# Performance work log

Hardware: AMD Instinct MI355X
Metric: run time of the kernel (lower is better)

Reference implementation:

```python
import jax, jax.numpy as jnp
import numpy as np
import math

B, T, H = 2, 1024, 2048
NH, NKV, HD = 8, 2, 256
S = 4           # altup_num_inputs
FF = 8192       # intermediate_size
LR = 64         # laurel_rank
EPS = 1e-6
ROPE_THETA = 1e6


def _ln(x, w):
    # Gemma3nRMSNorm in this repo: fp32 mean-subtract then F.layer_norm (no bias)
    x32 = x.astype(jnp.float32)
    xc = x32 - x32.mean(-1, keepdims=True)
    var = (xc * xc).mean(-1, keepdims=True)
    return (xc * jax.lax.rsqrt(var + EPS) * w.astype(jnp.float32)).astype(x.dtype)


def _rotate_half(x):
    x1, x2 = jnp.split(x, 2, axis=-1)
    return jnp.concatenate((-x2, x1), axis=-1)


def _rope(x, cos, sin):  # x: [B,nh,T,hd]; cos/sin: [B,T,hd]
    return x * cos[:, None] + _rotate_half(x) * sin[:, None]


def setup_inputs() -> dict:
    key = jax.random.key(0)
    ks = jax.random.split(key, 24)

    def w(k, shape, scale=0.02):
        return jax.random.normal(k, shape, jnp.float32) * scale

    hidden_states = jax.random.normal(ks[0], (S, B, T, H), jnp.float32)

    # real rotary embeddings
    inv_freq = 1.0 / (ROPE_THETA ** (np.arange(0, HD, 2, dtype=np.float64) / HD))
    freqs = np.arange(T, dtype=np.float64)[:, None] * inv_freq[None, :]
    emb = np.concatenate([freqs, freqs], axis=-1)  # [T,HD]
    cos = jnp.broadcast_to(jnp.asarray(np.cos(emb), jnp.float32)[None], (B, T, HD))
    sin = jnp.broadcast_to(jnp.asarray(np.sin(emb), jnp.float32)[None], (B, T, HD))

    return {
        "hidden_states": hidden_states, "cos": cos, "sin": sin,
        "wq": w(ks[1], (NH * HD, H)), "wk": w(ks[2], (NKV * HD, H)),
        "wv": w(ks[3], (NKV * HD, H)), "wo": w(ks[4], (H, NH * HD)),
        "q_norm_w": jnp.ones((HD,), jnp.float32), "k_norm_w": jnp.ones((HD,), jnp.float32),
        "input_ln_w": jnp.ones((H,), jnp.float32), "post_attn_ln_w": jnp.ones((H,), jnp.float32),
        "pre_ffw_ln_w": jnp.ones((H,), jnp.float32), "post_ffw_ln_w": jnp.ones((H,), jnp.float32),
        "gate_w": w(ks[5], (FF, H)), "up_w": w(ks[6], (FF, H)), "down_w": w(ks[7], (H, FF)),
        "laurel_left_w": w(ks[8], (LR, H)), "laurel_right_w": w(ks[9], (H, LR)),
        "laurel_norm_w": jnp.ones((H,), jnp.float32),
        "router_norm_w": jnp.ones((H,), jnp.float32),
        "router_w": w(ks[10], (S, H)),
        "pred_coef_w": w(ks[11], (S * S, S)),
        "corr_coef_w": w(ks[12], (S, S)),
        "correct_output_scale": w(ks[13], (H,), 1.0),
    }


def reference(hidden_states, cos, sin, wq, wk, wv, wo, q_norm_w, k_norm_w,
              input_ln_w, post_attn_ln_w, pre_ffw_ln_w, post_ffw_ln_w,
              gate_w, up_w, down_w, laurel_left_w, laurel_right_w, laurel_norm_w,
              router_norm_w, router_w, pred_coef_w, corr_coef_w, correct_output_scale):
    def modalities_of(x):  # router: RMSNorm -> scale -> linear -> tanh
        r = _ln(x, router_norm_w) * (1.0 / H)
        return jnp.tanh((r @ router_w.T).astype(jnp.float32)).astype(x.dtype)

    # ---- AltUp predict ----
    m = modalities_of(hidden_states[0])                      # [B,T,S]
    coefs = (m @ pred_coef_w.T).reshape(B, T, S, S)          # raw [B,T,S_out,S_in]
    # torch: matmul(h.permute(1,2,3,0), coefs.permute(0,1,3,2)) => sum_s h[s]*raw[...,j,s]
    predictions = jnp.einsum('sbth,btjs->jbth', hidden_states, coefs) + hidden_states

    active = predictions[0]
    x_norm = _ln(active, input_ln_w)

    # ---- Laurel block ----
    lau = (x_norm @ laurel_left_w.T) @ laurel_right_w.T
    laurel_out = x_norm + _ln(lau, laurel_norm_w)

    # ---- Attention (GQA, q/k/v norms, rope, scale=1.0) ----
    q = _ln((x_norm @ wq.T).reshape(B, T, NH, HD), q_norm_w).transpose(0, 2, 1, 3)
    q = _rope(q, cos, sin)
    k = _ln((x_norm @ wk.T).reshape(B, T, NKV, HD), k_norm_w).transpose(0, 2, 1, 3)
    k = _rope(k, cos, sin)
    v = _ln((x_norm @ wv.T).reshape(B, T, NKV, HD), jnp.ones((HD,), jnp.float32))
    v = v.transpose(0, 2, 1, 3)
    rep = NH // NKV
    k = jnp.repeat(k, rep, axis=1)
    v = jnp.repeat(v, rep, axis=1)
    scores = jnp.einsum('bhqd,bhkd->bhqk', q, k)             # scaling = 1.0 in Gemma3n
    causal = jnp.tril(jnp.ones((T, T), bool))
    scores = jnp.where(causal, scores, jnp.finfo(jnp.float32).min)
    attn = jax.nn.softmax(scores.astype(jnp.float32), axis=-1).astype(q.dtype)
    out = jnp.einsum('bhqk,bhkd->bhqd', attn, v)
    out = out.transpose(0, 2, 1, 3).reshape(B, T, NH * HD) @ wo.T
    out = _ln(out, post_attn_ln_w)

    attn_gated = active + out
    attn_laurel = (attn_gated + laurel_out) * (1.0 / math.sqrt(2.0))

    # ---- MLP (gelu-tanh gated) ----
    h = _ln(attn_laurel, pre_ffw_ln_w)
    ffw = (jax.nn.gelu(h @ gate_w.T, approximate=True) * (h @ up_w.T)) @ down_w.T
    ffw = _ln(ffw, post_ffw_ln_w)
    activated = attn_laurel + ffw

    # ---- AltUp correct ----
    mc = modalities_of(activated)                            # [B,T,S]
    innovation = activated - predictions[0]                  # [B,T,H]
    ccoefs = (mc @ corr_coef_w.T) + 1.0                      # [B,T,S]
    corrected = innovation[None] * ccoefs.transpose(2, 0, 1)[..., None] + predictions

    # scale_corrected_output on the active stream (altup_correct_scale=True)
    first = (corrected[0] * correct_output_scale).astype(corrected.dtype)
    corrected = corrected.at[0].set(first)
    return corrected
```

## Files before the change

kernel.cpp:

```cpp
#include <hip/hip_runtime.h>
#include <hip/hip_bf16.h>
#include <math.h>

#define B_   2
#define T_   1024
#define H_   2048
#define NH_  8
#define NKV_ 2
#define HD_  256
#define S_   4
#define FF_  8192
#define LR_  64
#define ROWS_ (B_*T_)
#define EPS_ 1e-6f

typedef __attribute__((ext_vector_type(8))) __bf16 bf16x8;
typedef __attribute__((ext_vector_type(4))) float floatx4;
typedef __attribute__((ext_vector_type(8))) unsigned short ushort8v;

__device__ __forceinline__ unsigned short f2bf(float f) {
    unsigned int u = __float_as_uint(f);
    return (unsigned short)((u + 0x7FFFu + ((u >> 16) & 1u)) >> 16);
}

__device__ __forceinline__ void gl_lds16(const void* g, void* l) {
    __builtin_amdgcn_global_load_lds(
        (const __attribute__((address_space(1))) void*)g,
        (__attribute__((address_space(3))) void*)l, 16, 0, 0);
}

__device__ __forceinline__ float block_sum(float v) {
    __shared__ float s4[4];
    #pragma unroll
    for (int o = 32; o > 0; o >>= 1) v += __shfl_down(v, o, 64);
    int lane = threadIdx.x & 63;
    int w    = threadIdx.x >> 6;
    __syncthreads();
    if (lane == 0) s4[w] = v;
    __syncthreads();
    return s4[0] + s4[1] + s4[2] + s4[3];
}

__device__ __forceinline__ float block_max(float v) {
    __shared__ float s4m[4];
    #pragma unroll
    for (int o = 32; o > 0; o >>= 1) v = fmaxf(v, __shfl_down(v, o, 64));
    int lane = threadIdx.x & 63;
    int w    = threadIdx.x >> 6;
    __syncthreads();
    if (lane == 0) s4m[w] = v;
    __syncthreads();
    return fmaxf(fmaxf(s4m[0], s4m[1]), fmaxf(s4m[2], s4m[3]));
}

__global__ __launch_bounds__(256) void cvt_bf16(
    const float* __restrict__ in, unsigned short* __restrict__ out, int n)
{
    int i = (blockIdx.x * 256 + threadIdx.x) * 8;
    if (i >= n) return;
    float4 v0 = *reinterpret_cast<const float4*>(in + i);
    float4 v1 = *reinterpret_cast<const float4*>(in + i + 4);
    ushort8v o;
    o[0] = f2bf(v0.x); o[1] = f2bf(v0.y); o[2] = f2bf(v0.z); o[3] = f2bf(v0.w);
    o[4] = f2bf(v1.x); o[5] = f2bf(v1.y); o[6] = f2bf(v1.z); o[7] = f2bf(v1.w);
    *reinterpret_cast<ushort8v*>(out + i) = o;
}

__global__ __launch_bounds__(256) void router_kernel(
    const float* __restrict__ x, const float* __restrict__ nw,
    const float* __restrict__ rw, float* __restrict__ mout)
{
    size_t row = blockIdx.x;
    int tid = threadIdx.x;
    const float* xr = x + row * H_;
    float v[8]; float s = 0.f;
    #pragma unroll
    for (int i = 0; i < 8; ++i) { v[i] = xr[i*256 + tid]; s += v[i]; }
    float mu = block_sum(s) * (1.f / H_);
    float ss = 0.f;
    #pragma unroll
    for (int i = 0; i < 8; ++i) { float c = v[i] - mu; ss += c * c; }
    float rstd = rsqrtf(block_sum(ss) * (1.f / H_) + EPS_);
    float n[8];
    #pragma unroll
    for (int i = 0; i < 8; ++i) n[i] = (v[i] - mu) * rstd * nw[i*256 + tid];
    for (int so = 0; so < S_; ++so) {
        float p = 0.f;
        #pragma unroll
        for (int i = 0; i < 8; ++i) p += n[i] * rw[(size_t)so * H_ + i*256 + tid];
        float dot = block_sum(p);
        if (tid == 0) mout[row * S_ + so] = tanhf(dot * (1.f / H_));
    }
}

__global__ __launch_bounds__(256) void predict_kernel(
    const float* __restrict__ hid, const float* __restrict__ m,
    const float* __restrict__ pcw, float* __restrict__ pred)
{
    size_t row = blockIdx.x;
    int tid = threadIdx.x;
    __shared__ float ms[4];
    __shared__ float c[16];
    if (tid < 4) ms[tid] = m[row * S_ + tid];
    __syncthreads();
    if (tid < 16) {
        float s = 0.f;
        #pragma unroll
        for (int i = 0; i < 4; ++i) s += ms[i] * pcw[tid * 4 + i];
        c[tid] = s;
    }
    __syncthreads();
    const size_t STRIDE = (size_t)ROWS_ * H_;
    #pragma unroll
    for (int i = 0; i < 8; ++i) {
        size_t idx = row * H_ + i*256 + tid;
        float h0 = hid[idx];
        float h1 = hid[idx + STRIDE];
        float h2 = hid[idx + 2*STRIDE];
        float h3 = hid[idx + 3*STRIDE];
        float hv[4] = {h0, h1, h2, h3};
        #pragma unroll
        for (int j = 0; j < 4; ++j) {
            float val = hv[j] + h0*c[j*4+0] + h1*c[j*4+1] + h2*c[j*4+2] + h3*c[j*4+3];
            pred[idx + (size_t)j * STRIDE] = val;
        }
    }
}

__global__ __launch_bounds__(256) void ln_residual(
    const float* __restrict__ x, const float* __restrict__ xadd,
    const float* __restrict__ w,
    const float* __restrict__ a1, const float* __restrict__ a2,
    float scale, float* __restrict__ out, unsigned short* __restrict__ outb)
{
    size_t row = blockIdx.x;
    int tid = threadIdx.x;
    const float* xr = x + row * H_;
    const float* xa = xadd ? xadd + row * H_ : nullptr;
    float v[8]; float s = 0.f;
    #pragma unroll
    for (int i = 0; i < 8; ++i) {
        v[i] = xr[i*256 + tid];
        if (xa) v[i] += xa[i*256 + tid];
        s += v[i];
    }
    float mu = block_sum(s) * (1.f / H_);
    float ss = 0.f;
    #pragma unroll
    for (int i = 0; i < 8; ++i) { float c = v[i] - mu; ss += c * c; }
    float rstd = rsqrtf(block_sum(ss) * (1.f / H_) + EPS_);
    #pragma unroll
    for (int i = 0; i < 8; ++i) {
        size_t idx = row * H_ + i*256 + tid;
        float y = (v[i] - mu) * rstd * w[i*256 + tid];
        if (a1) y += a1[idx];
        if (a2) y += a2[idx];
        y *= scale;
        if (out)  out[idx]  = y;
        if (outb) outb[idx] = f2bf(y);
    }
}

#define BM 64
#define BN 64
#define BK 32
#define LDP 68

__global__ __launch_bounds__(256) void gemm_nt(
    const float* __restrict__ A, const float* __restrict__ Bm,
    float* __restrict__ C, int M, int N, int K)
{
    __shared__ float As[BK][LDP];
    __shared__ float Bs[BK][LDP];
    int tid = threadIdx.x;
    int n0 = blockIdx.x * BN;
    int m0 = blockIdx.y * BM;
    int tx = tid & 15, ty = tid >> 4;
    int lrow = tid >> 3;
    int lk   = (tid & 7) << 2;
    float acc[4][4] = {};
    for (int k0 = 0; k0 < K; k0 += BK) {
        #pragma unroll
        for (int r = 0; r < 2; ++r) {
            int row = lrow + r * 32;
            float4 a4 = *reinterpret_cast<const float4*>(&A[(size_t)(m0 + row) * K + k0 + lk]);
            As[lk+0][row] = a4.x; As[lk+1][row] = a4.y; As[lk+2][row] = a4.z; As[lk+3][row] = a4.w;
            float4 b4 = *reinterpret_cast<const float4*>(&Bm[(size_t)(n0 + row) * K + k0 + lk]);
            Bs[lk+0][row] = b4.x; Bs[lk+1][row] = b4.y; Bs[lk+2][row] = b4.z; Bs[lk+3][row] = b4.w;
        }
        __syncthreads();
        #pragma unroll
        for (int k = 0; k < BK; ++k) {
            float4 av = *reinterpret_cast<const float4*>(&As[k][ty << 2]);
            float4 bv = *reinterpret_cast<const float4*>(&Bs[k][tx << 2]);
            float a[4] = {av.x, av.y, av.z, av.w};
            float b[4] = {bv.x, bv.y, bv.z, bv.w};
            #pragma unroll
            for (int i = 0; i < 4; ++i)
                #pragma unroll
                for (int j = 0; j < 4; ++j)
                    acc[i][j] = fmaf(a[i], b[j], acc[i][j]);
        }
        __syncthreads();
    }
    #pragma unroll
    for (int i = 0; i < 4; ++i) {
        float4 o; o.x = acc[i][0]; o.y = acc[i][1]; o.z = acc[i][2]; o.w = acc[i][3];
        *reinterpret_cast<float4*>(&C[(size_t)(m0 + (ty << 2) + i) * N + n0 + (tx << 2)]) = o;
    }
}

__global__ __launch_bounds__(256) void gemm_bf16nt(
    const unsigned short* __restrict__ A, const unsigned short* __restrict__ Bm,
    float* __restrict__ C, float* __restrict__ C2, int M, int N, int K)
{
    __shared__ unsigned short As[8192];
    __shared__ unsigned short Bs[8192];
    int tid = threadIdx.x;
    int lane = tid & 63;
    int wave = tid >> 6;
    int m0 = blockIdx.y * 128, n0 = blockIdx.x * 128;
    int Kper = K / gridDim.z;
    int kbeg = blockIdx.z * Kper;
    int kend = kbeg + Kper;
    int wm = (wave >> 1) * 64;
    int wn = (wave & 1) * 64;
    floatx4 acc[4][4] = {};

    const unsigned short* aG0 = A  + (size_t)(m0 + lane)      * K + wave * 8;
    const unsigned short* aG1 = A  + (size_t)(m0 + 64 + lane) * K + wave * 8;
    const unsigned short* bG0 = Bm + (size_t)(n0 + lane)      * K + wave * 8;
    const unsigned short* bG1 = Bm + (size_t)(n0 + 64 + lane) * K + wave * 8;

    int kc = lane >> 4, mr = lane & 15;

    {
        unsigned short* a = &As[wave * 1024];
        unsigned short* b = &Bs[wave * 1024];
        gl_lds16(aG0 + kbeg, a);
        gl_lds16(aG1 + kbeg, a + 512);
        gl_lds16(bG0 + kbeg, b);
        gl_lds16(bG1 + kbeg, b + 512);
    }
    __syncthreads();
    int cur = 0;
    for (int k0 = kbeg; k0 < kend; k0 += 32) {
        if (k0 + 32 < kend) {
            int nb = (cur ^ 1) * 4096;
            unsigned short* a = &As[nb + wave * 1024];
            unsigned short* b = &Bs[nb + wave * 1024];
            gl_lds16(aG0 + k0 + 32, a);
            gl_lds16(aG1 + k0 + 32, a + 512);
            gl_lds16(bG0 + k0 + 32, b);
            gl_lds16(bG1 + k0 + 32, b + 512);
        }
        int cb = cur * 4096;
        bf16x8 af[4], bfv[4];
        #pragma unroll
        for (int mi = 0; mi < 4; ++mi)
            af[mi] = *reinterpret_cast<const bf16x8*>(&As[cb + kc * 1024 + (wm + mi * 16 + mr) * 8]);
        #pragma unroll
        for (int ni = 0; ni < 4; ++ni)
            bfv[ni] = *reinterpret_cast<const bf16x8*>(&Bs[cb + kc * 1024 + (wn + ni * 16 + mr) * 8]);
        #pragma unroll
        for (int mi = 0; mi < 4; ++mi)
            #pragma unroll
            for (int ni = 0; ni < 4; ++ni)
                acc[mi][ni] = __builtin_amdgcn_mfma_f32_16x16x32_bf16(af[mi], bfv[ni], acc[mi][ni], 0, 0, 0);
        __syncthreads();
        cur ^= 1;
    }
    float* Cout = (blockIdx.z == 0) ? C : C2;
    int quad = lane >> 4;
    #pragma unroll
    for (int mi = 0; mi < 4; ++mi)
        #pragma unroll
        for (int ni = 0; ni < 4; ++ni)
            #pragma unroll
            for (int r = 0; r < 4; ++r)
                Cout[(size_t)(m0 + wm + mi * 16 + quad * 4 + r) * N + n0 + wn + ni * 16 + mr] = acc[mi][ni][r];
}

__global__ __launch_bounds__(256) void gemm_gateup_bf16(
    const unsigned short* __restrict__ A, const unsigned short* __restrict__ G,
    const unsigned short* __restrict__ U, unsigned short* __restrict__ Cbf,
    int M, int N, int K)
{
    __shared__ unsigned short As[8192];
    __shared__ unsigned short Gs[4096];
    __shared__ unsigned short Us[4096];
    int tid = threadIdx.x;
    int lane = tid & 63;
    int wave = tid >> 6;
    int m0 = blockIdx.y * 128, n0 = blockIdx.x * 64;
    floatx4 accg[2][4] = {};
    floatx4 accu[2][4] = {};

    const unsigned short* aG0 = A + (size_t)(m0 + lane)      * K + wave * 8;
    const unsigned short* aG1 = A + (size_t)(m0 + 64 + lane) * K + wave * 8;
    const unsigned short* gG  = G + (size_t)(n0 + lane)      * K + wave * 8;
    const unsigned short* uG  = U + (size_t)(n0 + lane)      * K + wave * 8;

    int kc = lane >> 4, mr = lane & 15;

    {
        gl_lds16(aG0, &As[wave * 1024]);
        gl_lds16(aG1, &As[wave * 1024 + 512]);
        gl_lds16(gG,  &Gs[wave * 512]);
        gl_lds16(uG,  &Us[wave * 512]);
    }
    __syncthreads();
    int cur = 0;
    for (int k0 = 0; k0 < K; k0 += 32) {
        if (k0 + 32 < K) {
            int a_nb = (cur ^ 1) * 4096;
            int g_nb = (cur ^ 1) * 2048;
            gl_lds16(aG0 + k0 + 32, &As[a_nb + wave * 1024]);
            gl_lds16(aG1 + k0 + 32, &As[a_nb + wave * 1024 + 512]);
            gl_lds16(gG + k0 + 32,  &Gs[g_nb + wave * 512]);
            gl_lds16(uG + k0 + 32,  &Us[g_nb + wave * 512]);
        }
        int ab = cur * 4096, gb = cur * 2048;
        bf16x8 af[2], gf[4], uf[4];
        #pragma unroll
        for (int mi = 0; mi < 2; ++mi)
            af[mi] = *reinterpret_cast<const bf16x8*>(&As[ab + kc * 1024 + (wave * 32 + mi * 16 + mr) * 8]);
        #pragma unroll
        for (int ni = 0; ni < 4; ++ni) {
            gf[ni] = *reinterpret_cast<const bf16x8*>(&Gs[gb + kc * 512 + (ni * 16 + mr) * 8]);
            uf[ni] = *reinterpret_cast<const bf16x8*>(&Us[gb + kc * 512 + (ni * 16 + mr) * 8]);
        }
        #pragma unroll
        for (int mi = 0; mi < 2; ++mi)
            #pragma unroll
            for (int ni = 0; ni < 4; ++ni) {
                accg[mi][ni] = __builtin_amdgcn_mfma_f32_16x16x32_bf16(af[mi], gf[ni], accg[mi][ni], 0, 0, 0);
                accu[mi][ni] = __builtin_amdgcn_mfma_f32_16x16x32_bf16(af[mi], uf[ni], accu[mi][ni], 0, 0, 0);
            }
        __syncthreads();
        cur ^= 1;
    }
    int quad = lane >> 4;
    #pragma unroll
    for (int mi = 0; mi < 2; ++mi) {
        int rb = m0 + wave * 32 + mi * 16 + quad * 4;
        #pragma unroll
        for (int ni = 0; ni < 4; ++ni)
            #pragma unroll
            for (int r = 0; r < 4; ++r) {
                float g = accg[mi][ni][r];
                float gl = 0.5f * g * (1.f + tanhf(0.7978845608028654f * (g + 0.044715f * g * g * g)));
                float val = gl * accu[mi][ni][r];
                Cbf[(size_t)(rb + r) * N + n0 + ni * 16 + mr] = f2bf(val);
            }
    }
}

__global__ __launch_bounds__(256) void qkv_norm_rope_fused(
    const float* __restrict__ in, const float* __restrict__ qw,
    const float* __restrict__ kw,
    const float* __restrict__ cs, const float* __restrict__ sn,
    unsigned short* __restrict__ qo, unsigned short* __restrict__ ko,
    unsigned short* __restrict__ vo)
{
    int blk = blockIdx.x;
    int hh = blk % 12;
    int trow = blk / 12;
    int b = trow / T_;
    int t = trow % T_;
    int d = threadIdx.x;
    float x = in[(size_t)trow * 3072 + hh * HD_ + d];
    float mu = block_sum(x) * (1.f / HD_);
    float xc = x - mu;
    float var = block_sum(xc * xc) * (1.f / HD_);
    float wv_ = (hh < 8) ? qw[d] : (hh < 10 ? kw[d] : 1.f);
    float n = xc * rsqrtf(var + EPS_) * wv_;
    __shared__ float buf[HD_];
    buf[d] = n;
    __syncthreads();
    float val = n;
    if (hh < 10) {
        float c = cs[(size_t)trow * HD_ + d];
        float s = sn[(size_t)trow * HD_ + d];
        float other = (d < 128) ? -buf[d + 128] : buf[d - 128];
        val = n * c + other * s;
    }
    if (hh < 8)
        qo[(((size_t)b * NH_ + hh) * T_ + t) * HD_ + d] = f2bf(val);
    else if (hh < 10)
        ko[(((size_t)b * NKV_ + (hh - 8)) * T_ + t) * HD_ + d] = f2bf(val);
    else
        vo[(((size_t)b * NKV_ + (hh - 10)) * HD_ + d) * T_ + t] = f2bf(val);
}

__global__ __launch_bounds__(256) void qk_gemm(
    const unsigned short* __restrict__ Q, const unsigned short* __restrict__ Kt,
    float* __restrict__ S, int head_base)
{
    if (blockIdx.x > blockIdx.y) return;
    int z = blockIdx.z;
    int bh = head_base + z;
    const unsigned short* A  = Q  + (size_t)bh * T_ * HD_;
    const unsigned short* Bm = Kt + (size_t)(bh >> 2) * T_ * HD_;
    float* C = S + (size_t)z * T_ * T_;

    __shared__ unsigned short As[8192];
    __shared__ unsigned short Bs[8192];
    int tid = threadIdx.x;
    int lane = tid & 63;
    int wave = tid >> 6;
    int m0 = blockIdx.y * 128, n0 = blockIdx.x * 128;
    int wm = (wave >> 1) * 64;
    int wn = (wave & 1) * 64;
    floatx4 acc[4][4] = {};

    const unsigned short* aG0 = A  + (size_t)(m0 + lane)      * HD_ + wave * 8;
    const unsigned short* aG1 = A  + (size_t)(m0 + 64 + lane) * HD_ + wave * 8;
    const unsigned short* bG0 = Bm + (size_t)(n0 + lane)      * HD_ + wave * 8;
    const unsigned short* bG1 = Bm + (size_t)(n0 + 64 + lane) * HD_ + wave * 8;

    int kc = lane >> 4, mr = lane & 15;

    {
        gl_lds16(aG0, &As[wave * 1024]);
        gl_lds16(aG1, &As[wave * 1024 + 512]);
        gl_lds16(bG0, &Bs[wave * 1024]);
        gl_lds16(bG1, &Bs[wave * 1024 + 512]);
    }
    __syncthreads();
    int cur = 0;
    for (int k0 = 0; k0 < HD_; k0 += 32) {
        if (k0 + 32 < HD_) {
            int nb = (cur ^ 1) * 4096;
            gl_lds16(aG0 + k0 + 32, &As[nb + wave * 1024]);
            gl_lds16(aG1 + k0 + 32, &As[nb + wave * 1024 + 512]);
            gl_lds16(bG0 + k0 + 32, &Bs[nb + wave * 1024]);
            gl_lds16(bG1 + k0 + 32, &Bs[nb + wave * 1024 + 512]);
        }
        int cb = cur * 4096;
        bf16x8 af[4], bfv[4];
        #pragma unroll
        for (int mi = 0; mi < 4; ++mi)
            af[mi] = *reinterpret_cast<const bf16x8*>(&As[cb + kc * 1024 + (wm + mi * 16 + mr) * 8]);
        #pragma unroll
        for (int ni = 0; ni < 4; ++ni)
            bfv[ni] = *reinterpret_cast<const bf16x8*>(&Bs[cb + kc * 1024 + (wn + ni * 16 + mr) * 8]);
        #pragma unroll
        for (int mi = 0; mi < 4; ++mi)
            #pragma unroll
            for (int ni = 0; ni < 4; ++ni)
                acc[mi][ni] = __builtin_amdgcn_mfma_f32_16x16x32_bf16(af[mi], bfv[ni], acc[mi][ni], 0, 0, 0);
        __syncthreads();
        cur ^= 1;
    }
    int quad = lane >> 4;
    #pragma unroll
    for (int mi = 0; mi < 4; ++mi)
        #pragma unroll
        for (int ni = 0; ni < 4; ++ni)
            #pragma unroll
            for (int r = 0; r < 4; ++r)
                C[(size_t)(m0 + wm + mi * 16 + quad * 4 + r) * T_ + n0 + wn + ni * 16 + mr] = acc[mi][ni][r];
}

__global__ __launch_bounds__(256) void softmax_causal(
    const float* __restrict__ S, unsigned short* __restrict__ P)
{
    int qi = blockIdx.x;
    int g  = blockIdx.y;
    int tid = threadIdx.x;
    int L = qi + 1;
    const float* Srow = S + ((size_t)g * T_ + qi) * T_;
    unsigned short* Prow = P + ((size_t)g * T_ + qi) * T_;
    float v[4];
    float mx = -3.402823466e38f;
    #pragma unroll
    for (int i = 0; i < 4; ++i) {
        int idx = i * 256 + tid;
        v[i] = (idx < L) ? Srow[idx] : -3.402823466e38f;
        mx = fmaxf(mx, v[i]);
    }
    mx = block_max(mx);
    float sm = 0.f;
    float e[4];
    #pragma unroll
    for (int i = 0; i < 4; ++i) {
        int idx = i * 256 + tid;
        e[i] = (idx < L) ? expf(v[i] - mx) : 0.f;
        sm += e[i];
    }
    sm = block_sum(sm);
    float inv = 1.f / sm;
    #pragma unroll
    for (int i = 0; i < 4; ++i)
        Prow[i * 256 + tid] = f2bf(e[i] * inv);
}

__global__ __launch_bounds__(256) void pv_gemm(
    const unsigned short* __restrict__ P, const unsigned short* __restrict__ Vt,
    unsigned short* __restrict__ Out)
{
    int z = blockIdx.z;
    int b = z >> 3;
    int h = z & 7;
    const unsigned short* A  = P  + (size_t)z * T_ * T_;
    const unsigned short* Bm = Vt + (size_t)(z >> 2) * HD_ * T_;

    __shared__ unsigned short As[8192];
    __shared__ unsigned short Bs[8192];
    int tid = threadIdx.x;
    int lane = tid & 63;
    int wave = tid >> 6;
    int m0 = blockIdx.y * 128, n0 = blockIdx.x * 128;
    int Kend = m0 + 128;
    int wm = (wave >> 1) * 64;
    int wn = (wave & 1) * 64;
    floatx4 acc[4][4] = {};

    const unsigned short* aG0 = A  + (size_t)(m0 + lane)      * T_ + wave * 8;
    const unsigned short* aG1 = A  + (size_t)(m0 + 64 + lane) * T_ + wave * 8;
    const unsigned short* bG0 = Bm + (size_t)(n0 + lane)      * T_ + wave * 8;
    const unsigned short* bG1 = Bm + (size_t)(n0 + 64 + lane) * T_ + wave * 8;

    int kc = lane >> 4, mr = lane & 15;

    {
        gl_lds16(aG0, &As[wave * 1024]);
        gl_lds16(aG1, &As[wave * 1024 + 512]);
        gl_lds16(bG0, &Bs[wave * 1024]);
        gl_lds16(bG1, &Bs[wave * 1024 + 512]);
    }
    __syncthreads();
    int cur = 0;
    for (int k0 = 0; k0 < Kend; k0 += 32) {
        if (k0 + 32 < Kend) {
            int nb = (cur ^ 1) * 4096;
            gl_lds16(aG0 + k0 + 32, &As[nb + wave * 1024]);
            gl_lds16(aG1 + k0 + 32, &As[nb + wave * 1024 + 512]);
            gl_lds16(bG0 + k0 + 32, &Bs[nb + wave * 1024]);
            gl_lds16(bG1 + k0 + 32, &Bs[nb + wave * 1024 + 512]);
        }
        int cb = cur * 4096;
        bf16x8 af[4], bfv[4];
        #pragma unroll
        for (int mi = 0; mi < 4; ++mi)
            af[mi] = *reinterpret_cast<const bf16x8*>(&As[cb + kc * 1024 + (wm + mi * 16 + mr) * 8]);
        #pragma unroll
        for (int ni = 0; ni < 4; ++ni)
            bfv[ni] = *reinterpret_cast<const bf16x8*>(&Bs[cb + kc * 1024 + (wn + ni * 16 + mr) * 8]);
        #pragma unroll
        for (int mi = 0; mi < 4; ++mi)
            #pragma unroll
            for (int ni = 0; ni < 4; ++ni)
                acc[mi][ni] = __builtin_amdgcn_mfma_f32_16x16x32_bf16(af[mi], bfv[ni], acc[mi][ni], 0, 0, 0);
        __syncthreads();
        cur ^= 1;
    }
    int quad = lane >> 4;
    #pragma unroll
    for (int mi = 0; mi < 4; ++mi)
        #pragma unroll
        for (int ni = 0; ni < 4; ++ni)
            #pragma unroll
            for (int r = 0; r < 4; ++r) {
                int row = m0 + wm + mi * 16 + quad * 4 + r;
                int col = n0 + wn + ni * 16 + mr;
                Out[((size_t)(b * T_ + row)) * (NH_ * HD_) + h * HD_ + col] =
                    f2bf(acc[mi][ni][r]);
            }
}

__global__ __launch_bounds__(256) void correct_kernel(
    const float* __restrict__ act, const float* __restrict__ pred,
    const float* __restrict__ mc, const float* __restrict__ ccw,
    const float* __restrict__ cscale, float* __restrict__ out)
{
    size_t row = blockIdx.x;
    int tid = threadIdx.x;
    __shared__ float ms[4];
    __shared__ float cc[4];
    if (tid < 4) ms[tid] = mc[row * S_ + tid];
    __syncthreads();
    if (tid < 4) {
        float s = 1.f;
        #pragma unroll
        for (int i = 0; i < 4; ++i) s += ms[i] * ccw[tid * 4 + i];
        cc[tid] = s;
    }
    __syncthreads();
    const size_t STRIDE = (size_t)ROWS_ * H_;
    #pragma unroll
    for (int i = 0; i < 8; ++i) {
        size_t idx = row * H_ + i*256 + tid;
        float a  = act[idx];
        float p0 = pred[idx];
        float inn = a - p0;
        #pragma unroll
        for (int j = 0; j < 4; ++j) {
            float val = inn * cc[j] + pred[idx + (size_t)j * STRIDE];
            if (j == 0) val *= cscale[i*256 + tid];
            out[idx + (size_t)j * STRIDE] = val;
        }
    }
}

extern "C" void kernel_launch(void* const* d_in, const int* in_sizes, int n_in,
                              void* d_out, int out_size, void* d_ws, size_t ws_size,
                              hipStream_t stream)
{
    (void)in_sizes; (void)n_in; (void)out_size; (void)ws_size;
    const float* hidden         = (const float*)d_in[0];
    const float* cosp           = (const float*)d_in[1];
    const float* sinp           = (const float*)d_in[2];
    const float* wq             = (const float*)d_in[3];
    const float* wk             = (const float*)d_in[4];
    const float* wv             = (const float*)d_in[5];
    const float* wo             = (const float*)d_in[6];
    const float* q_norm_w       = (const float*)d_in[7];
    const float* k_norm_w       = (const float*)d_in[8];
    const float* input_ln_w     = (const float*)d_in[9];
    const float* post_attn_ln_w = (const float*)d_in[10];
    const float* pre_ffw_ln_w   = (const float*)d_in[11];
    const float* post_ffw_ln_w  = (const float*)d_in[12];
    const float* gate_w         = (const float*)d_in[13];
    const float* up_w           = (const float*)d_in[14];
    const float* down_w         = (const float*)d_in[15];
    const float* ll_w           = (const float*)d_in[16];
    const float* lr_w           = (const float*)d_in[17];
    const float* laurel_norm_w  = (const float*)d_in[18];
    const float* router_norm_w  = (const float*)d_in[19];
    const float* router_w       = (const float*)d_in[20];
    const float* pred_coef_w    = (const float*)d_in[21];
    const float* corr_coef_w    = (const float*)d_in[22];
    const float* cscale         = (const float*)d_in[23];
    float* outp = (float*)d_out;

    char* base = (char*)d_ws;
    float* pred   = (float*)base;              base += 67108864;
    float* xnorm  = (float*)base;              base += 16777216;
    unsigned short* xnorm_bf = (unsigned short*)base; base += 8388608;
    float* lout   = (float*)base;              base += 16777216;
    float* alaur  = (float*)base;              base += 16777216;
    float* tmpH   = (float*)base;              base += 16777216;
    float* mbuf   = (float*)base;              base += 32768;
    float* mcbuf  = (float*)base;              base += 32768;
    float* ltmp   = (float*)base;              base += 524288;
    char* arena = base;
    unsigned short* qkvw_bf = (unsigned short*)arena;
    float* qkv_pre = (float*)(arena + 12582912);
    unsigned short* Pbuf    = (unsigned short*)arena;
    unsigned short* q_bf    = (unsigned short*)(arena + 37748736);
    unsigned short* k_bf    = (unsigned short*)(arena + 46137344);
    unsigned short* vT_bf   = (unsigned short*)(arena + 48234496);
    unsigned short* attn_bf = (unsigned short*)(arena + 50331648);
    unsigned short* wo_bf   = (unsigned short*)(arena + 58720256);
    float* Sbuf             = (float*)(arena + 67108864);
    unsigned short* gate_bf = (unsigned short*)arena;
    unsigned short* up_bf   = (unsigned short*)(arena + 33554432);
    unsigned short* gu_bf   = (unsigned short*)(arena + 67108864);
    unsigned short* down_bf = gate_bf;
    float* activated = lout;

    router_kernel <<<ROWS_, 256, 0, stream>>>(hidden, router_norm_w, router_w, mbuf);
    predict_kernel<<<ROWS_, 256, 0, stream>>>(hidden, mbuf, pred_coef_w, pred);
    ln_residual   <<<ROWS_, 256, 0, stream>>>(pred, nullptr, input_ln_w, nullptr, nullptr, 1.f, xnorm, xnorm_bf);

    gemm_nt<<<dim3(LR_/BN, ROWS_/BM), 256, 0, stream>>>(xnorm, ll_w, ltmp, ROWS_, LR_, H_);
    gemm_nt<<<dim3(H_/BN,  ROWS_/BM), 256, 0, stream>>>(ltmp, lr_w, tmpH, ROWS_, H_, LR_);
    ln_residual<<<ROWS_, 256, 0, stream>>>(tmpH, nullptr, laurel_norm_w, xnorm, nullptr, 1.f, lout, nullptr);

    cvt_bf16<<<2048, 256, 0, stream>>>(wq, qkvw_bf,            4194304);
    cvt_bf16<<< 512, 256, 0, stream>>>(wk, qkvw_bf + 4194304,  1048576);
    cvt_bf16<<< 512, 256, 0, stream>>>(wv, qkvw_bf + 5242880,  1048576);
    gemm_bf16nt<<<dim3(24, 16, 1), 256, 0, stream>>>(xnorm_bf, qkvw_bf, qkv_pre, nullptr, ROWS_, 3072, H_);
    qkv_norm_rope_fused<<<ROWS_*12, 256, 0, stream>>>(qkv_pre, q_norm_w, k_norm_w, cosp, sinp, q_bf, k_bf, vT_bf);
    cvt_bf16<<<2048, 256, 0, stream>>>(wo, wo_bf, 4194304);
    for (int hb = 0; hb < B_ * NH_; hb += 8) {
        qk_gemm       <<<dim3(8, 8, 8), 256, 0, stream>>>(q_bf, k_bf, Sbuf, hb);
        softmax_causal<<<dim3(T_, 8),   256, 0, stream>>>(Sbuf, Pbuf + (size_t)hb * T_ * T_);
    }
    pv_gemm<<<dim3(2, 8, 16), 256, 0, stream>>>(Pbuf, vT_bf, attn_bf);
    gemm_bf16nt<<<dim3(16, 16, 2), 256, 0, stream>>>(attn_bf, wo_bf, tmpH, xnorm, ROWS_, H_, NH_*HD_);
    ln_residual<<<ROWS_, 256, 0, stream>>>(tmpH, xnorm, post_attn_ln_w, pred, lout, 0.7071067811865475f, alaur, nullptr);

    ln_residual<<<ROWS_, 256, 0, stream>>>(alaur, nullptr, pre_ffw_ln_w, nullptr, nullptr, 1.f, nullptr, xnorm_bf);
    cvt_bf16<<<8192, 256, 0, stream>>>(gate_w, gate_bf, 16777216);
    cvt_bf16<<<8192, 256, 0, stream>>>(up_w,   up_bf,   16777216);
    gemm_gateup_bf16<<<dim3(128, 16), 256, 0, stream>>>(xnorm_bf, gate_bf, up_bf, gu_bf, ROWS_, FF_, H_);
    cvt_bf16<<<8192, 256, 0, stream>>>(down_w, down_bf, 16777216);
    gemm_bf16nt<<<dim3(16, 16, 2), 256, 0, stream>>>(gu_bf, down_bf, tmpH, xnorm, ROWS_, H_, FF_);
    ln_residual<<<ROWS_, 256, 0, stream>>>(tmpH, xnorm, post_ffw_ln_w, alaur, nullptr, 1.f, activated, nullptr);

    router_kernel <<<ROWS_, 256, 0, stream>>>(activated, router_norm_w, router_w, mcbuf);
    correct_kernel<<<ROWS_, 256, 0, stream>>>(activated, pred, mcbuf, corr_coef_w, cscale, outp);
}
```

Measured before the change: 1.183 ms.

## Coalesce global-to-LDS loads with row-major K tiles; widen gate/up GEMM tile

Each GEMM's global-to-LDS loader now reads four consecutive 16-byte chunks of a row per four lanes, where before each lane read a different row. The LDS tile is stored row-major with 32 K-elements per row, and the fragment reads are re-indexed to match. The gate/up GEMM tile grows from 128x64 to 128x128 with a 2x2 wave layout, doubling accumulators per thread and halving the grid. This targets uncoalesced global loads and redundant A-tile reads, at the risk of LDS bank conflicts from the 64-byte row stride and higher register pressure in the gate/up kernel.

Result: faster. 1.116 ms (-5.7%).

```diff
diff --git a/kernel.cpp b/kernel.cpp
--- a/kernel.cpp
+++ b/kernel.cpp
@@ -227,41 +227,37 @@
     int wn = (wave & 1) * 64;
     floatx4 acc[4][4] = {};
 
-    const unsigned short* aG0 = A  + (size_t)(m0 + lane)      * K + wave * 8;
-    const unsigned short* aG1 = A  + (size_t)(m0 + 64 + lane) * K + wave * 8;
-    const unsigned short* bG0 = Bm + (size_t)(n0 + lane)      * K + wave * 8;
-    const unsigned short* bG1 = Bm + (size_t)(n0 + 64 + lane) * K + wave * 8;
+    int lr = lane >> 2;
+    int lc = lane & 3;
+    const unsigned short* aG0 = A  + (size_t)(m0 + wave*16 + lr) * K + lc * 8;
+    const unsigned short* aG1 = aG0 + (size_t)64 * K;
+    const unsigned short* bG0 = Bm + (size_t)(n0 + wave*16 + lr) * K + lc * 8;
+    const unsigned short* bG1 = bG0 + (size_t)64 * K;
 
     int kc = lane >> 4, mr = lane & 15;
 
-    {
-        unsigned short* a = &As[wave * 1024];
-        unsigned short* b = &Bs[wave * 1024];
-        gl_lds16(aG0 + kbeg, a);
-        gl_lds16(aG1 + kbeg, a + 512);
-        gl_lds16(bG0 + kbeg, b);
-        gl_lds16(bG1 + kbeg, b + 512);
-    }
+    gl_lds16(aG0 + kbeg, &As[wave * 512]);
+    gl_lds16(aG1 + kbeg, &As[2048 + wave * 512]);
+    gl_lds16(bG0 + kbeg, &Bs[wave * 512]);
+    gl_lds16(bG1 + kbeg, &Bs[2048 + wave * 512]);
     __syncthreads();
     int cur = 0;
     for (int k0 = kbeg; k0 < kend; k0 += 32) {
         if (k0 + 32 < kend) {
             int nb = (cur ^ 1) * 4096;
-            unsigned short* a = &As[nb + wave * 1024];
-            unsigned short* b = &Bs[nb + wave * 1024];
-            gl_lds16(aG0 + k0 + 32, a);
-            gl_lds16(aG1 + k0 + 32, a + 512);
-            gl_lds16(bG0 + k0 + 32, b);
-            gl_lds16(bG1 + k0 + 32, b + 512);
+            gl_lds16(aG0 + k0 + 32, &As[nb + wave * 512]);
+            gl_lds16(aG1 + k0 + 32, &As[nb + 2048 + wave * 512]);
+            gl_lds16(bG0 + k0 + 32, &Bs[nb + wave * 512]);
+            gl_lds16(bG1 + k0 + 32, &Bs[nb + 2048 + wave * 512]);
         }
         int cb = cur * 4096;
         bf16x8 af[4], bfv[4];
         #pragma unroll
         for (int mi = 0; mi < 4; ++mi)
-            af[mi] = *reinterpret_cast<const bf16x8*>(&As[cb + kc * 1024 + (wm + mi * 16 + mr) * 8]);
+            af[mi] = *reinterpret_cast<const bf16x8*>(&As[cb + (wm + mi * 16 + mr) * 32 + kc * 8]);
         #pragma unroll
         for (int ni = 0; ni < 4; ++ni)
-            bfv[ni] = *reinterpret_cast<const bf16x8*>(&Bs[cb + kc * 1024 + (wn + ni * 16 + mr) * 8]);
+            bfv[ni] = *reinterpret_cast<const bf16x8*>(&Bs[cb + (wn + ni * 16 + mr) * 32 + kc * 8]);
         #pragma unroll
         for (int mi = 0; mi < 4; ++mi)
             #pragma unroll
@@ -287,51 +283,58 @@
     int M, int N, int K)
 {
     __shared__ unsigned short As[8192];
-    __shared__ unsigned short Gs[4096];
-    __shared__ unsigned short Us[4096];
+    __shared__ unsigned short Gs[8192];
+    __shared__ unsigned short Us[8192];
     int tid = threadIdx.x;
     int lane = tid & 63;
     int wave = tid >> 6;
-    int m0 = blockIdx.y * 128, n0 = blockIdx.x * 64;
-    floatx4 accg[2][4] = {};
-    floatx4 accu[2][4] = {};
-
-    const unsigned short* aG0 = A + (size_t)(m0 + lane)      * K + wave * 8;
-    const unsigned short* aG1 = A + (size_t)(m0 + 64 + lane) * K + wave * 8;
-    const unsigned short* gG  = G + (size_t)(n0 + lane)      * K + wave * 8;
-    const unsigned short* uG  = U + (size_t)(n0 + lane)      * K + wave * 8;
+    int m0 = blockIdx.y * 128, n0 = blockIdx.x * 128;
+    int wm  = (wave >> 1) * 64;
+    int wnf = (wave & 1) * 64;
+    floatx4 accg[4][4] = {};
+    floatx4 accu[4][4] = {};
+
+    int lr = lane >> 2;
+    int lc = lane & 3;
+    const unsigned short* aG0 = A + (size_t)(m0 + wave*16 + lr) * K + lc * 8;
+    const unsigned short* aG1 = aG0 + (size_t)64 * K;
+    const unsigned short* gG0 = G + (size_t)(n0 + wave*16 + lr) * K + lc * 8;
+    const unsigned short* gG1 = gG0 + (size_t)64 * K;
+    const unsigned short* uG0 = U + (size_t)(n0 + wave*16 + lr) * K + lc * 8;
+    const unsigned short* uG1 = uG0 + (size_t)64 * K;
 
     int kc = lane >> 4, mr = lane & 15;
 
-    {
-        gl_lds16(aG0, &As[wave * 1024]);
-        gl_lds16(aG1, &As[wave * 1024 + 512]);
-        gl_lds16(gG,  &Gs[wave * 512]);
-        gl_lds16(uG,  &Us[wave * 512]);
-    }
+    gl_lds16(aG0, &As[wave * 512]);
+    gl_lds16(aG1, &As[2048 + wave * 512]);
+    gl_lds16(gG0, &Gs[wave * 512]);
+    gl_lds16(gG1, &Gs[2048 + wave * 512]);
+    gl_lds16(uG0, &Us[wave * 512]);
+    gl_lds16(uG1, &Us[2048 + wave * 512]);
     __syncthreads();
     int cur = 0;
     for (int k0 = 0; k0 < K; k0 += 32) {
         if (k0 + 32 < K) {
-            int a_nb = (cur ^ 1) * 4096;
-            int g_nb = (cur ^ 1) * 2048;
-            gl_lds16(aG0 + k0 + 32, &As[a_nb + wave * 1024]);
-            gl_lds16(aG1 + k0 + 32, &As[a_nb + wave * 1024 + 512]);
-            gl_lds16(gG + k0 + 32,  &Gs[g_nb + wave * 512]);
-            gl_lds16(uG + k0 + 32,  &Us[g_nb + wave * 512]);
-        }
-        int ab = cur * 4096, gb = cur * 2048;
-        bf16x8 af[2], gf[4], uf[4];
-        #pragma unroll
-        for (int mi = 0; mi < 2; ++mi)
-            af[mi] = *reinterpret_cast<const bf16x8*>(&As[ab + kc * 1024 + (wave * 32 + mi * 16 + mr) * 8]);
+            int nb = (cur ^ 1) * 4096;
+            gl_lds16(aG0 + k0 + 32, &As[nb + wave * 512]);
+            gl_lds16(aG1 + k0 + 32, &As[nb + 2048 + wave * 512]);
+            gl_lds16(gG0 + k0 + 32, &Gs[nb + wave * 512]);
+            gl_lds16(gG1 + k0 + 32, &Gs[nb + 2048 + wave * 512]);
+            gl_lds16(uG0 + k0 + 32, &Us[nb + wave * 512]);
+            gl_lds16(uG1 + k0 + 32, &Us[nb + 2048 + wave * 512]);
+        }
+        int cb = cur * 4096;
+        bf16x8 af[4], gf[4], uf[4];
+        #pragma unroll
+        for (int mi = 0; mi < 4; ++mi)
+            af[mi] = *reinterpret_cast<const bf16x8*>(&As[cb + (wm + mi * 16 + mr) * 32 + kc * 8]);
         #pragma unroll
         for (int ni = 0; ni < 4; ++ni) {
-            gf[ni] = *reinterpret_cast<const bf16x8*>(&Gs[gb + kc * 512 + (ni * 16 + mr) * 8]);
-            uf[ni] = *reinterpret_cast<const bf16x8*>(&Us[gb + kc * 512 + (ni * 16 + mr) * 8]);
-        }
-        #pragma unroll
-        for (int mi = 0; mi < 2; ++mi)
+            gf[ni] = *reinterpret_cast<const bf16x8*>(&Gs[cb + (wnf + ni * 16 + mr) * 32 + kc * 8]);
+            uf[ni] = *reinterpret_cast<const bf16x8*>(&Us[cb + (wnf + ni * 16 + mr) * 32 + kc * 8]);
+        }
+        #pragma unroll
+        for (int mi = 0; mi < 4; ++mi)
             #pragma unroll
             for (int ni = 0; ni < 4; ++ni) {
                 accg[mi][ni] = __builtin_amdgcn_mfma_f32_16x16x32_bf16(af[mi], gf[ni], accg[mi][ni], 0, 0, 0);
@@ -342,8 +345,8 @@
     }
     int quad = lane >> 4;
     #pragma unroll
-    for (int mi = 0; mi < 2; ++mi) {
-        int rb = m0 + wave * 32 + mi * 16 + quad * 4;
+    for (int mi = 0; mi < 4; ++mi) {
+        int rb = m0 + wm + mi * 16 + quad * 4;
         #pragma unroll
         for (int ni = 0; ni < 4; ++ni)
             #pragma unroll
@@ -351,7 +354,7 @@
                 float g = accg[mi][ni][r];
                 float gl = 0.5f * g * (1.f + tanhf(0.7978845608028654f * (g + 0.044715f * g * g * g)));
                 float val = gl * accu[mi][ni][r];
-                Cbf[(size_t)(rb + r) * N + n0 + ni * 16 + mr] = f2bf(val);
+                Cbf[(size_t)(rb + r) * N + n0 + wnf + ni * 16 + mr] = f2bf(val);
             }
     }
 }
@@ -414,37 +417,37 @@
     int wn = (wave & 1) * 64;
     floatx4 acc[4][4] = {};
 
-    const unsigned short* aG0 = A  + (size_t)(m0 + lane)      * HD_ + wave * 8;
-    const unsigned short* aG1 = A  + (size_t)(m0 + 64 + lane) * HD_ + wave * 8;
-    const unsigned short* bG0 = Bm + (size_t)(n0 + lane)      * HD_ + wave * 8;
-    const unsigned short* bG1 = Bm + (size_t)(n0 + 64 + lane) * HD_ + wave * 8;
+    int lr = lane >> 2;
+    int lc = lane & 3;
+    const unsigned short* aG0 = A  + (size_t)(m0 + wave*16 + lr) * HD_ + lc * 8;
+    const unsigned short* aG1 = aG0 + (size_t)64 * HD_;
+    const unsigned short* bG0 = Bm + (size_t)(n0 + wave*16 + lr) * HD_ + lc * 8;
+    const unsigned short* bG1 = bG0 + (size_t)64 * HD_;
 
     int kc = lane >> 4, mr = lane & 15;
 
-    {
-        gl_lds16(aG0, &As[wave * 1024]);
-        gl_lds16(aG1, &As[wave * 1024 + 512]);
-        gl_lds16(bG0, &Bs[wave * 1024]);
-        gl_lds16(bG1, &Bs[wave * 1024 + 512]);
-    }
+    gl_lds16(aG0, &As[wave * 512]);
+    gl_lds16(aG1, &As[2048 + wave * 512]);
+    gl_lds16(bG0, &Bs[wave * 512]);
+    gl_lds16(bG1, &Bs[2048 + wave * 512]);
     __syncthreads();
     int cur = 0;
     for (int k0 = 0; k0 < HD_; k0 += 32) {
         if (k0 + 32 < HD_) {
             int nb = (cur ^ 1) * 4096;
-            gl_lds16(aG0 + k0 + 32, &As[nb + wave * 1024]);
-            gl_lds16(aG1 + k0 + 32, &As[nb + wave * 1024 + 512]);
-            gl_lds16(bG0 + k0 + 32, &Bs[nb + wave * 1024]);
-            gl_lds16(bG1 + k0 + 32, &Bs[nb + wave * 1024 + 512]);
+            gl_lds16(aG0 + k0 + 32, &As[nb + wave * 512]);
+            gl_lds16(aG1 + k0 + 32, &As[nb + 2048 + wave * 512]);
+            gl_lds16(bG0 + k0 + 32, &Bs[nb + wave * 512]);
+            gl_lds16(bG1 + k0 + 32, &Bs[nb + 2048 + wave * 512]);
         }
         int cb = cur * 4096;
         bf16x8 af[4], bfv[4];
         #pragma unroll
         for (int mi = 0; mi < 4; ++mi)
-            af[mi] = *reinterpret_cast<const bf16x8*>(&As[cb + kc * 1024 + (wm + mi * 16 + mr) * 8]);
+            af[mi] = *reinterpret_cast<const bf16x8*>(&As[cb + (wm + mi * 16 + mr) * 32 + kc * 8]);
         #pragma unroll
         for (int ni = 0; ni < 4; ++ni)
-            bfv[ni] = *reinterpret_cast<const bf16x8*>(&Bs[cb + kc * 1024 + (wn + ni * 16 + mr) * 8]);
+            bfv[ni] = *reinterpret_cast<const bf16x8*>(&Bs[cb + (wn + ni * 16 + mr) * 32 + kc * 8]);
         #pragma unroll
         for (int mi = 0; mi < 4; ++mi)
             #pragma unroll
@@ -517,37 +520,37 @@
     int wn = (wave & 1) * 64;
     floatx4 acc[4][4] = {};
 
-    const unsigned short* aG0 = A  + (size_t)(m0 + lane)      * T_ + wave * 8;
-    const unsigned short* aG1 = A  + (size_t)(m0 + 64 + lane) * T_ + wave * 8;
-    const unsigned short* bG0 = Bm + (size_t)(n0 + lane)      * T_ + wave * 8;
-    const unsigned short* bG1 = Bm + (size_t)(n0 + 64 + lane) * T_ + wave * 8;
+    int lr = lane >> 2;
+    int lc = lane & 3;
+    const unsigned short* aG0 = A  + (size_t)(m0 + wave*16 + lr) * T_ + lc * 8;
+    const unsigned short* aG1 = aG0 + (size_t)64 * T_;
+    const unsigned short* bG0 = Bm + (size_t)(n0 + wave*16 + lr) * T_ + lc * 8;
+    const unsigned short* bG1 = bG0 + (size_t)64 * T_;
 
     int kc = lane >> 4, mr = lane & 15;
 
-    {
-        gl_lds16(aG0, &As[wave * 1024]);
-        gl_lds16(aG1, &As[wave * 1024 + 512]);
-        gl_lds16(bG0, &Bs[wave * 1024]);
-        gl_lds16(bG1, &Bs[wave * 1024 + 512]);
-    }
+    gl_lds16(aG0, &As[wave * 512]);
+    gl_lds16(aG1, &As[2048 + wave * 512]);
+    gl_lds16(bG0, &Bs[wave * 512]);
+    gl_lds16(bG1, &Bs[2048 + wave * 512]);
     __syncthreads();
     int cur = 0;
     for (int k0 = 0; k0 < Kend; k0 += 32) {
         if (k0 + 32 < Kend) {
             int nb = (cur ^ 1) * 4096;
-            gl_lds16(aG0 + k0 + 32, &As[nb + wave * 1024]);
-            gl_lds16(aG1 + k0 + 32, &As[nb + wave * 1024 + 512]);
-            gl_lds16(bG0 + k0 + 32, &Bs[nb + wave * 1024]);
-            gl_lds16(bG1 + k0 + 32, &Bs[nb + wave * 1024 + 512]);
+            gl_lds16(aG0 + k0 + 32, &As[nb + wave * 512]);
+            gl_lds16(aG1 + k0 + 32, &As[nb + 2048 + wave * 512]);
+            gl_lds16(bG0 + k0 + 32, &Bs[nb + wave * 512]);
+            gl_lds16(bG1 + k0 + 32, &Bs[nb + 2048 + wave * 512]);
         }
         int cb = cur * 4096;
         bf16x8 af[4], bfv[4];
         #pragma unroll
         for (int mi = 0; mi < 4; ++mi)
-            af[mi] = *reinterpret_cast<const bf16x8*>(&As[cb + kc * 1024 + (wm + mi * 16 + mr) * 8]);
+            af[mi] = *reinterpret_cast<const bf16x8*>(&As[cb + (wm + mi * 16 + mr) * 32 + kc * 8]);
         #pragma unroll
         for (int ni = 0; ni < 4; ++ni)
-            bfv[ni] = *reinterpret_cast<const bf16x8*>(&Bs[cb + kc * 1024 + (wn + ni * 16 + mr) * 8]);
+            bfv[ni] = *reinterpret_cast<const bf16x8*>(&Bs[cb + (wn + ni * 16 + mr) * 32 + kc * 8]);
         #pragma unroll
         for (int mi = 0; mi < 4; ++mi)
             #pragma unroll
@@ -686,7 +689,7 @@
     ln_residual<<<ROWS_, 256, 0, stream>>>(alaur, nullptr, pre_ffw_ln_w, nullptr, nullptr, 1.f, nullptr, xnorm_bf);
     cvt_bf16<<<8192, 256, 0, stream>>>(gate_w, gate_bf, 16777216);
     cvt_bf16<<<8192, 256, 0, stream>>>(up_w,   up_bf,   16777216);
-    gemm_gateup_bf16<<<dim3(128, 16), 256, 0, stream>>>(xnorm_bf, gate_bf, up_bf, gu_bf, ROWS_, FF_, H_);
+    gemm_gateup_bf16<<<dim3(64, 16), 256, 0, stream>>>(xnorm_bf, gate_bf, up_bf, gu_bf, ROWS_, FF_, H_);
     cvt_bf16<<<8192, 256, 0, stream>>>(down_w, down_bf, 16777216);
     gemm_bf16nt<<<dim3(16, 16, 2), 256, 0, stream>>>(gu_bf, down_bf, tmpH, xnorm, ROWS_, H_, FF_);
     ln_residual<<<ROWS_, 256, 0, stream>>>(tmpH, xnorm, post_ffw_ln_w, alaur, nullptr, 1.f, activated, nullptr);
```
